# Optimization experiments

Hardware: AMD Instinct MI355X
Metric: run time of the kernel (lower is better)

The kernel has to match this reference:

```python
import jax, jax.numpy as jnp
import numpy as np

N, H = 131072, 256          # rows, hidden_dim
P, K_OCC, K_SUBJ = 16, 8, 16  # phases, occurrences per phase, subjects per occurrence
O = P * K_OCC               # 128 total occurrence classes
S = O * K_SUBJ              # 2048 total subject classes


def setup_inputs() -> dict:
    key = jax.random.key(0)
    ks = jax.random.split(key, 10)
    X = jax.random.normal(ks[0], (N, H), jnp.float32)
    X_phase = jax.random.randint(ks[1], (N,), 0, P)
    X_occ_local = jax.random.randint(ks[2], (N,), 0, K_OCC)
    X_subj_local = jax.random.randint(ks[3], (N,), 0, K_SUBJ)
    sc = 1.0 / np.sqrt(H)  # nn.Linear default init range
    W_phase = jax.random.uniform(ks[4], (P, H), jnp.float32, -sc, sc)
    b_phase = jax.random.uniform(ks[5], (P,), jnp.float32, -sc, sc)
    W_p2o = jax.random.uniform(ks[6], (O, H), jnp.float32, -sc, sc)      # stacked phase_to_occurrence Linears
    b_p2o = jax.random.uniform(ks[7], (O,), jnp.float32, -sc, sc)
    W_o2s = jax.random.uniform(ks[8], (S, H), jnp.float32, -sc, sc)      # stacked occurrence_to_subj Linears
    b_o2s = jax.random.uniform(ks[9], (S,), jnp.float32, -sc, sc)
    return {
        "X": X, "W_phase": W_phase, "b_phase": b_phase,
        "W_p2o": W_p2o, "b_p2o": b_p2o, "W_o2s": W_o2s, "b_o2s": b_o2s,
        "X_phase": X_phase, "X_occ_local": X_occ_local, "X_subj_local": X_subj_local,
    }


def reference(X, W_phase, b_phase, W_p2o, b_p2o, W_o2s, b_o2s,
              X_phase, X_occ_local, X_subj_local):
    n = X.shape[0]
    rows = jnp.arange(n)

    # phase head: softmax over all P phases, pick the true phase prob
    phase_proba = jax.nn.softmax(X @ W_phase.T + b_phase, axis=1)[rows, X_phase]  # [N]

    # occurrence head: per-sample small Linear chosen by phase key -> compute all
    # stacked logits once, gather the phase's K_OCC-block, softmax within block
    occ_logits = (X @ W_p2o.T + b_p2o).reshape(n, P, K_OCC)[rows, X_phase]        # [N, K_OCC]
    occ_proba = jax.nn.softmax(occ_logits, axis=1)[rows, X_occ_local]             # [N]

    # subject head: same pattern keyed by global occurrence id
    X_occurrence = X_phase * K_OCC + X_occ_local                                   # global occ ids
    subj_logits = (X @ W_o2s.T + b_o2s).reshape(n, O, K_SUBJ)[rows, X_occurrence]  # [N, K_SUBJ]
    subj_proba = jax.nn.softmax(subj_logits, axis=1)[rows, X_subj_local]           # [N]

    po = phase_proba * occ_proba
    return (phase_proba, po, po * subj_proba)
```

## Files before the change

### kernel.cpp

```cpp
#include <hip/hip_runtime.h>

#define H_ 256
#define P_ 16
#define KOCC 8
#define KSUBJ 16
#define O_ 128
#define CAPMAX 2048

typedef __attribute__((ext_vector_type(8))) __bf16 bf16x8;
typedef __attribute__((ext_vector_type(4))) float f32x4;

__device__ __forceinline__ bf16x8 load_bf8(const float* p) {
  float4 a = *(const float4*)p;
  float4 b = *(const float4*)(p + 4);
  bf16x8 r;
  r[0] = (__bf16)a.x; r[1] = (__bf16)a.y; r[2] = (__bf16)a.z; r[3] = (__bf16)a.w;
  r[4] = (__bf16)b.x; r[5] = (__bf16)b.y; r[6] = (__bf16)b.z; r[7] = (__bf16)b.w;
  return r;
}

__device__ __forceinline__ float rmax16(float v) {
  v = fmaxf(v, __shfl_xor(v, 1));
  v = fmaxf(v, __shfl_xor(v, 2));
  v = fmaxf(v, __shfl_xor(v, 4));
  v = fmaxf(v, __shfl_xor(v, 8));
  return v;
}
__device__ __forceinline__ float rsum16(float v) {
  v += __shfl_xor(v, 1);
  v += __shfl_xor(v, 2);
  v += __shfl_xor(v, 4);
  v += __shfl_xor(v, 8);
  return v;
}

__global__ __launch_bounds__(512) void scatter_kernel(
    const int* __restrict__ xp, const int* __restrict__ xo,
    int* counts, int* brows, int n, int cap) {
  __shared__ int hist[O_];
  __shared__ int basev[O_];
  int tid = threadIdx.x;
  if (tid < O_) hist[tid] = 0;
  __syncthreads();
  int i = blockIdx.x * blockDim.x + tid;
  int b = 0, pos = -1;
  if (i < n) {
    b = xp[i] * KOCC + xo[i];
    pos = atomicAdd(&hist[b], 1);
  }
  __syncthreads();
  if (tid < O_) basev[tid] = atomicAdd(&counts[tid], hist[tid]);
  __syncthreads();
  if (pos >= 0) {
    int idx = basev[b] + pos;
    if (idx < cap) brows[b * cap + idx] = i;
  }
}

__global__ __launch_bounds__(256) void hsm_main(
    const float* __restrict__ X,
    const float* __restrict__ Wp, const float* __restrict__ bp,
    const float* __restrict__ Wo, const float* __restrict__ bo,
    const float* __restrict__ Ws, const float* __restrict__ bs,
    const int* __restrict__ subj,
    const int* __restrict__ counts, const int* __restrict__ brows,
    float* __restrict__ out, int n, int cap) {
  int b = blockIdx.x >> 3;
  int chunk = blockIdx.x & 7;
  int count = counts[b];
  if (count > cap) count = cap;
  int start = chunk * 256;
  if (start >= count) return;
  int p = b >> 3;
  int occl = b & 7;
  int lane = threadIdx.x & 63;
  int wave = threadIdx.x >> 6;
  int col = lane & 15;
  int quad = lane >> 4;

  const float* w0 = Wp + col * H_;
  const float* w1 = Wo + (p * KOCC + (col & 7)) * H_;
  const float* w2 = Ws + (b * KSUBJ + col) * H_;
  bf16x8 bf0[8], bf1[8], bf2[8];
#pragma unroll
  for (int kk = 0; kk < 8; ++kk) {
    int off = kk * 32 + quad * 8;
    bf0[kk] = load_bf8(w0 + off);
    bf1[kk] = load_bf8(w1 + off);
    bf2[kk] = load_bf8(w2 + off);
  }
  bool v1 = col < KOCC;
  float bias0 = bp[col];
  float bias1 = v1 ? bo[p * KOCC + col] : 0.0f;
  float bias2 = bs[b * KSUBJ + col];

  const int* brow_b = brows + b * cap;

  for (int g = 0; g < 4; ++g) {
    int base = start + wave * 64 + g * 16;
    if (base >= count) break;
    int rem = count - base;
    int ra_idx = base + (col < rem ? col : rem - 1);
    int rida = brow_b[ra_idx];
    const float* xr = X + (size_t)rida * H_;
    f32x4 acc0 = {0.f, 0.f, 0.f, 0.f};
    f32x4 acc1 = {0.f, 0.f, 0.f, 0.f};
    f32x4 acc2 = {0.f, 0.f, 0.f, 0.f};
#pragma unroll
    for (int kk = 0; kk < 8; ++kk) {
      bf16x8 a = load_bf8(xr + kk * 32 + quad * 8);
      acc0 = __builtin_amdgcn_mfma_f32_16x16x32_bf16(a, bf0[kk], acc0, 0, 0, 0);
      acc1 = __builtin_amdgcn_mfma_f32_16x16x32_bf16(a, bf1[kk], acc1, 0, 0, 0);
      acc2 = __builtin_amdgcn_mfma_f32_16x16x32_bf16(a, bf2[kk], acc2, 0, 0, 0);
    }
#pragma unroll
    for (int r = 0; r < 4; ++r) {
      int rloc = quad * 4 + r;
      bool rv = rloc < rem;
      int ridr = brow_b[base + (rv ? rloc : 0)];
      int tsub = subj[ridr];
      float l0 = acc0[r] + bias0;
      float m0 = rmax16(l0);
      float e0 = __expf(l0 - m0);
      float s0 = rsum16(e0);
      float p0 = __shfl(e0, quad * 16 + p) / s0;
      float l1 = v1 ? (acc1[r] + bias1) : -3.0e38f;
      float m1 = rmax16(l1);
      float e1 = v1 ? __expf(l1 - m1) : 0.0f;
      float s1 = rsum16(e1);
      float p1 = __shfl(e1, quad * 16 + occl) / s1;
      float l2 = acc2[r] + bias2;
      float m2 = rmax16(l2);
      float e2 = __expf(l2 - m2);
      float s2 = rsum16(e2);
      float p2 = __shfl(e2, quad * 16 + tsub) / s2;
      if (col == 0 && rv) {
        float po = p0 * p1;
        out[ridr] = p0;
        out[n + ridr] = po;
        out[2 * n + ridr] = po * p2;
      }
    }
  }
}

extern "C" void kernel_launch(void* const* d_in, const int* in_sizes, int n_in,
                              void* d_out, int out_size, void* d_ws, size_t ws_size,
                              hipStream_t stream) {
  const float* X  = (const float*)d_in[0];
  const float* Wp = (const float*)d_in[1];
  const float* bp = (const float*)d_in[2];
  const float* Wo = (const float*)d_in[3];
  const float* bo = (const float*)d_in[4];
  const float* Ws = (const float*)d_in[5];
  const float* bs = (const float*)d_in[6];
  const int* xp   = (const int*)d_in[7];
  const int* xo   = (const int*)d_in[8];
  const int* xs   = (const int*)d_in[9];
  float* out = (float*)d_out;
  int n = in_sizes[7];

  int* wsI = (int*)d_ws;
  int* counts = wsI;
  int* brows = wsI + 128;
  long avail = (long)(ws_size / 4) - 128;
  int cap = (int)(avail / O_);
  if (cap > CAPMAX) cap = CAPMAX;
  if (cap < 1) cap = 1;

  hipMemsetAsync(counts, 0, O_ * sizeof(int), stream);
  scatter_kernel<<<dim3((n + 511) / 512), dim3(512), 0, stream>>>(xp, xo, counts, brows, n, cap);
  hsm_main<<<dim3(O_ * 8), dim3(256), 0, stream>>>(X, Wp, bp, Wo, bo, Ws, bs, xs,
                                                   counts, brows, out, n, cap);
}
```

Baseline: 266.3 us.

## Stage bf16 weight fragments in LDS, split rows finer, batch scatter

The main kernel now uses 32 blocks per occurrence bucket of 64 rows each, so every wave handles one 16-row tile instead of looping over four, which gives far more blocks to fill the GPU. Weight fragments for the three heads are converted to bf16 once per block into shared memory instead of being held in registers per wave. Row ids and subject labels are fetched once and broadcast with shuffles rather than reloaded per output row. The scatter kernel handles 4096 rows per 1024-thread block to cut global counter atomics. The cost is re-converting the weights in every one of the many smaller blocks, plus an extra barrier.

```diff
diff --git a/kernel.cpp b/kernel.cpp
--- a/kernel.cpp
+++ b/kernel.cpp
@@ -34,7 +34,7 @@
   return v;
 }
 
-__global__ __launch_bounds__(512) void scatter_kernel(
+__global__ __launch_bounds__(1024) void scatter_kernel(
     const int* __restrict__ xp, const int* __restrict__ xo,
     int* counts, int* brows, int n, int cap) {
   __shared__ int hist[O_];
@@ -42,18 +42,26 @@
   int tid = threadIdx.x;
   if (tid < O_) hist[tid] = 0;
   __syncthreads();
-  int i = blockIdx.x * blockDim.x + tid;
-  int b = 0, pos = -1;
-  if (i < n) {
-    b = xp[i] * KOCC + xo[i];
-    pos = atomicAdd(&hist[b], 1);
+  int base_i = blockIdx.x * 4096 + tid;
+  int be[4], pos[4];
+#pragma unroll
+  for (int e = 0; e < 4; ++e) {
+    int i = base_i + e * 1024;
+    pos[e] = -1;
+    if (i < n) {
+      be[e] = xp[i] * KOCC + xo[i];
+      pos[e] = atomicAdd(&hist[be[e]], 1);
+    }
   }
   __syncthreads();
   if (tid < O_) basev[tid] = atomicAdd(&counts[tid], hist[tid]);
   __syncthreads();
-  if (pos >= 0) {
-    int idx = basev[b] + pos;
-    if (idx < cap) brows[b * cap + idx] = i;
+#pragma unroll
+  for (int e = 0; e < 4; ++e) {
+    if (pos[e] >= 0) {
+      int idx = basev[be[e]] + pos[e];
+      if (idx < cap) brows[be[e] * cap + idx] = base_i + e * 1024;
+    }
   }
 }
 
@@ -65,81 +73,92 @@
     const int* __restrict__ subj,
     const int* __restrict__ counts, const int* __restrict__ brows,
     float* __restrict__ out, int n, int cap) {
-  int b = blockIdx.x >> 3;
-  int chunk = blockIdx.x & 7;
+  int b = blockIdx.x >> 5;
+  int chunk = blockIdx.x & 31;
   int count = counts[b];
   if (count > cap) count = cap;
-  int start = chunk * 256;
+  int start = chunk * 64;
   if (start >= count) return;
   int p = b >> 3;
   int occl = b & 7;
+
+  __shared__ __bf16 Bf[3 * 8 * 64 * 8];
+  {
+    int t = threadIdx.x;
+#pragma unroll
+    for (int it = 0; it < 6; ++it) {
+      int fid = it * 256 + t;
+      int lane_f = fid & 63;
+      int hk = fid >> 6;
+      int head = hk >> 3, kk = hk & 7;
+      int colf = lane_f & 15, quadf = lane_f >> 4;
+      const float* src;
+      if (head == 0)      src = Wp + colf * H_;
+      else if (head == 1) src = Wo + (p * KOCC + (colf & 7)) * H_;
+      else                src = Ws + (b * KSUBJ + colf) * H_;
+      bf16x8 v = load_bf8(src + kk * 32 + quadf * 8);
+      *(bf16x8*)&Bf[(size_t)fid * 8] = v;
+    }
+  }
+  __syncthreads();
+
   int lane = threadIdx.x & 63;
   int wave = threadIdx.x >> 6;
   int col = lane & 15;
   int quad = lane >> 4;
 
-  const float* w0 = Wp + col * H_;
-  const float* w1 = Wo + (p * KOCC + (col & 7)) * H_;
-  const float* w2 = Ws + (b * KSUBJ + col) * H_;
-  bf16x8 bf0[8], bf1[8], bf2[8];
-#pragma unroll
-  for (int kk = 0; kk < 8; ++kk) {
-    int off = kk * 32 + quad * 8;
-    bf0[kk] = load_bf8(w0 + off);
-    bf1[kk] = load_bf8(w1 + off);
-    bf2[kk] = load_bf8(w2 + off);
-  }
+  int base = start + wave * 16;
+  if (base >= count) return;
+  int rem = count - base;
+
   bool v1 = col < KOCC;
   float bias0 = bp[col];
   float bias1 = v1 ? bo[p * KOCC + col] : 0.0f;
   float bias2 = bs[b * KSUBJ + col];
 
   const int* brow_b = brows + b * cap;
+  int rida = brow_b[base + (col < rem ? col : rem - 1)];
+  int subjv = subj[rida];
+  const float* xr = X + (size_t)rida * H_;
 
-  for (int g = 0; g < 4; ++g) {
-    int base = start + wave * 64 + g * 16;
-    if (base >= count) break;
-    int rem = count - base;
-    int ra_idx = base + (col < rem ? col : rem - 1);
-    int rida = brow_b[ra_idx];
-    const float* xr = X + (size_t)rida * H_;
-    f32x4 acc0 = {0.f, 0.f, 0.f, 0.f};
-    f32x4 acc1 = {0.f, 0.f, 0.f, 0.f};
-    f32x4 acc2 = {0.f, 0.f, 0.f, 0.f};
+  const bf16x8* Bfrag = (const bf16x8*)Bf;
+  f32x4 acc0 = {0.f, 0.f, 0.f, 0.f};
+  f32x4 acc1 = {0.f, 0.f, 0.f, 0.f};
+  f32x4 acc2 = {0.f, 0.f, 0.f, 0.f};
 #pragma unroll
-    for (int kk = 0; kk < 8; ++kk) {
-      bf16x8 a = load_bf8(xr + kk * 32 + quad * 8);
-      acc0 = __builtin_amdgcn_mfma_f32_16x16x32_bf16(a, bf0[kk], acc0, 0, 0, 0);
-      acc1 = __builtin_amdgcn_mfma_f32_16x16x32_bf16(a, bf1[kk], acc1, 0, 0, 0);
-      acc2 = __builtin_amdgcn_mfma_f32_16x16x32_bf16(a, bf2[kk], acc2, 0, 0, 0);
-    }
+  for (int kk = 0; kk < 8; ++kk) {
+    bf16x8 a = load_bf8(xr + kk * 32 + quad * 8);
+    acc0 = __builtin_amdgcn_mfma_f32_16x16x32_bf16(a, Bfrag[kk * 64 + lane], acc0, 0, 0, 0);
+    acc1 = __builtin_amdgcn_mfma_f32_16x16x32_bf16(a, Bfrag[(8 + kk) * 64 + lane], acc1, 0, 0, 0);
+    acc2 = __builtin_amdgcn_mfma_f32_16x16x32_bf16(a, Bfrag[(16 + kk) * 64 + lane], acc2, 0, 0, 0);
+  }
+
 #pragma unroll
-    for (int r = 0; r < 4; ++r) {
-      int rloc = quad * 4 + r;
-      bool rv = rloc < rem;
-      int ridr = brow_b[base + (rv ? rloc : 0)];
-      int tsub = subj[ridr];
-      float l0 = acc0[r] + bias0;
-      float m0 = rmax16(l0);
-      float e0 = __expf(l0 - m0);
-      float s0 = rsum16(e0);
-      float p0 = __shfl(e0, quad * 16 + p) / s0;
-      float l1 = v1 ? (acc1[r] + bias1) : -3.0e38f;
-      float m1 = rmax16(l1);
-      float e1 = v1 ? __expf(l1 - m1) : 0.0f;
-      float s1 = rsum16(e1);
-      float p1 = __shfl(e1, quad * 16 + occl) / s1;
-      float l2 = acc2[r] + bias2;
-      float m2 = rmax16(l2);
-      float e2 = __expf(l2 - m2);
-      float s2 = rsum16(e2);
-      float p2 = __shfl(e2, quad * 16 + tsub) / s2;
-      if (col == 0 && rv) {
-        float po = p0 * p1;
-        out[ridr] = p0;
-        out[n + ridr] = po;
-        out[2 * n + ridr] = po * p2;
-      }
+  for (int r = 0; r < 4; ++r) {
+    int rloc = quad * 4 + r;
+    bool rv = rloc < rem;
+    int ridr = __shfl(rida, rloc);
+    int tsub = __shfl(subjv, rloc);
+    float l0 = acc0[r] + bias0;
+    float m0 = rmax16(l0);
+    float e0 = __expf(l0 - m0);
+    float s0 = rsum16(e0);
+    float p0 = __shfl(e0, quad * 16 + p) / s0;
+    float l1 = v1 ? (acc1[r] + bias1) : -3.0e38f;
+    float m1 = rmax16(l1);
+    float e1 = v1 ? __expf(l1 - m1) : 0.0f;
+    float s1 = rsum16(e1);
+    float p1 = __shfl(e1, quad * 16 + occl) / s1;
+    float l2 = acc2[r] + bias2;
+    float m2 = rmax16(l2);
+    float e2 = __expf(l2 - m2);
+    float s2 = rsum16(e2);
+    float p2 = __shfl(e2, quad * 16 + tsub) / s2;
+    if (col == 0 && rv) {
+      float po = p0 * p1;
+      out[ridr] = p0;
+      out[n + ridr] = po;
+      out[2 * n + ridr] = po * p2;
     }
   }
 }
@@ -169,7 +188,7 @@
   if (cap < 1) cap = 1;
 
   hipMemsetAsync(counts, 0, O_ * sizeof(int), stream);
-  scatter_kernel<<<dim3((n + 511) / 512), dim3(512), 0, stream>>>(xp, xo, counts, brows, n, cap);
-  hsm_main<<<dim3(O_ * 8), dim3(256), 0, stream>>>(X, Wp, bp, Wo, bo, Ws, bs, xs,
-                                                   counts, brows, out, n, cap);
+  scatter_kernel<<<dim3((n + 4095) / 4096), dim3(1024), 0, stream>>>(xp, xo, counts, brows, n, cap);
+  hsm_main<<<dim3(O_ * 32), dim3(256), 0, stream>>>(X, Wp, bp, Wo, bo, Ws, bs, xs,
+                                                    counts, brows, out, n, cap);
 }
```

Result: faster. 245.5 us (-7.8%).
